# Kernel optimization log

Hardware: AMD Instinct MI355X
Metric: run time of the kernel (lower is better)

## Reference

```python
import jax, jax.numpy as jnp
import numpy as np

B, T, S = 64, 256, 512          # batch, decode steps, source length
IN, H, P, C = 512, 512, 256, 512  # in_size, rnn hidden, ctx_proj_size, ctx_size


def setup_inputs() -> dict:
    key = jax.random.key(0)
    ks = jax.random.split(key, 10)
    def n(k, sh, s=0.05):
        return jax.random.normal(k, sh, dtype=jnp.float32) * s
    return {
        "dec_input": n(ks[0], (B, T, IN), 1.0),
        "ctx": n(ks[1], (B, S, C), 1.0),
        "ctx_mask": jnp.ones((B, S), jnp.float32),
        # LSTMCell layer 0: input = in_size + ctx_proj_size (input feeding)
        "Wih0": n(ks[2], (4 * H, IN + P)),
        "Whh0": n(ks[3], (4 * H, H)),
        "bih0": jnp.zeros((4 * H,), jnp.float32),
        "bhh0": jnp.zeros((4 * H,), jnp.float32),
        # LSTMCell layer 1
        "Wih1": n(ks[4], (4 * H, H)),
        "Whh1": n(ks[5], (4 * H, H)),
        "bih1": jnp.zeros((4 * H,), jnp.float32),
        "bhh1": jnp.zeros((4 * H,), jnp.float32),
        # bilinear (Luong general) attention weight
        "Watt": n(ks[6], (H, C)),
        # ctx projection: Linear(rnn_size + att.out_features -> ctx_proj_size)
        "Wproj": n(ks[7], (P, H + C)),
        "bproj": jnp.zeros((P,), jnp.float32),
    }


def _lstm_cell(x, h, c, Wih, Whh, bih, bhh):
    # PyTorch LSTMCell gate order: i, f, g, o
    g = x @ Wih.T + bih + h @ Whh.T + bhh
    i, f, gg, o = jnp.split(g, 4, axis=-1)
    c_new = jax.nn.sigmoid(f) * c + jax.nn.sigmoid(i) * jnp.tanh(gg)
    h_new = jax.nn.sigmoid(o) * jnp.tanh(c_new)
    return h_new, c_new


def reference(dec_input, ctx, ctx_mask, Wih0, Whh0, bih0, bhh0,
              Wih1, Whh1, bih1, bhh1, Watt, Wproj, bproj):
    Bn = dec_input.shape[0]
    neg = (ctx_mask - 1.0) * 1e9  # additive mask: 0 where valid, -1e9 where pad

    def step(carry, x_t):
        h0, c0, h1, c1, feed = carry
        # input feeding at layer 0
        x = jnp.concatenate([x_t, feed], axis=1)
        h0, c0 = _lstm_cell(x, h0, c0, Wih0, Whh0, bih0, bhh0)
        h1, c1 = _lstm_cell(h0, h1, c1, Wih1, Whh1, bih1, bhh1)
        # attention on last layer (att_nth_layer == -1)
        q = h1 @ Watt                                   # [B, C]
        score = jnp.einsum('bc,bsc->bs', q, ctx) + neg  # [B, S]
        alpha = jax.nn.softmax(score, axis=-1)
        ectx = jnp.einsum('bs,bsc->bc', alpha, ctx)     # expected context [B, C]
        # ctx projection with tanh (scale_src = scale_tgt = 1.0)
        res = jnp.tanh(jnp.concatenate([h1, ectx], axis=1) @ Wproj.T + bproj)
        return (h0, c0, h1, c1, res), (res, alpha)

    z = lambda d: jnp.zeros((Bn, d), jnp.float32)
    init = (z(H), z(H), z(H), z(H), z(P))
    _, (dec_out, att_w) = jax.lax.scan(step, init, jnp.swapaxes(dec_input, 0, 1))
    # dec_output [B, T, P], attention weights [B, T, S]
    return jnp.swapaxes(dec_out, 0, 1), jnp.swapaxes(att_w, 0, 1)
```

## Files before the change

kernel.cpp:

```cpp
#include <hip/hip_runtime.h>
#include <math.h>

#define B  64
#define T  256
#define S  512
#define IN 512
#define H  512
#define P  256
#define C  512

typedef _Float16 f16x8 __attribute__((ext_vector_type(8)));
typedef float    f32x4 __attribute__((ext_vector_type(4)));
typedef unsigned short u16x8 __attribute__((ext_vector_type(8)));

#define MFMA16(a, b, c) __builtin_amdgcn_mfma_f32_16x16x32_f16(a, b, c, 0, 0, 0)

#define O_C0      0
#define O_C1      131072
#define O_H0F0    262144
#define O_H0F1    393216
#define O_H1F0    524288
#define O_H1F1    655360
#define O_FEEDF   786432
#define O_H1F32   851968
#define O_XF0     983040
#define O_XF1     1114112
#define O_Q       1245184
#define O_PS      1376256
#define O_PSP     1378304
#define O_PEA     1509376
#define O_BCAT0   2557952
#define O_BCAT1   2566144
#define O_WPROJT  2574336
#define O_W0F     3622912
#define O_W1F     14108672
#define O_WATTF   22497280
#define O_CTXH    23545856

__device__ __forceinline__ float sigm(float x) { return 1.f / (1.f + __expf(-x)); }

__device__ __forceinline__ void split2(float v, unsigned short& hi, unsigned short& lo)
{
    _Float16 h = (_Float16)v;
    float r = (v - (float)h) * 4096.f;
    _Float16 l2 = (_Float16)r;
    union { _Float16 f; unsigned short u; } a, b2;
    a.f = h; b2.f = l2;
    hi = a.u; lo = b2.u;
}

__device__ __forceinline__ unsigned short f2h(float v)
{
    union { _Float16 f; unsigned short u; } x;
    x.f = (_Float16)v;
    return x.u;
}

__device__ __forceinline__ float h2f(unsigned short u)
{
    union { unsigned short u; _Float16 f; } x;
    x.u = u;
    return (float)x.f;
}

__device__ __forceinline__ int frag_us(int r, int k)
{
    return ((((k >> 5) * 4 + (r >> 4)) * 64 + ((k >> 3) & 3) * 16 + (r & 15)) * 16) + (k & 7);
}

__device__ __forceinline__ void gemm_core(
    const unsigned short* A0, int n0, const unsigned short* A1, int n1,
    const unsigned short* A2, const unsigned short* Wf, int nks, int ct,
    float* red, int tid)
{
    const int l = tid & 63, kh = tid >> 6;
    f32x4 acch[4] = {};
    f32x4 accl[4] = {};
    const int KQ = nks >> 3;
#pragma unroll 2
    for (int i = 0; i < KQ; ++i) {
        const int ks = kh * KQ + i;
        const unsigned short* ap; int ksl;
        if (ks < n0)           { ap = A0; ksl = ks; }
        else if (ks < n0 + n1) { ap = A1; ksl = ks - n0; }
        else                   { ap = A2; ksl = ks - n0 - n1; }
        const f16x8* bp = (const f16x8*)(Wf + ((long)(ct * nks + ks) * 64 + l) * 16);
        const f16x8 bh = bp[0];
        const f16x8 bl = bp[1];
#pragma unroll
        for (int mt = 0; mt < 4; ++mt) {
            const f16x8* app = (const f16x8*)(ap + (((ksl * 4 + mt) * 64 + l) * 16));
            const f16x8 ah = app[0];
            const f16x8 al = app[1];
            acch[mt] = MFMA16(ah, bh, acch[mt]);
            accl[mt] = MFMA16(ah, bl, accl[mt]);
            accl[mt] = MFMA16(al, bh, accl[mt]);
        }
    }
#pragma unroll
    for (int mt = 0; mt < 4; ++mt) {
        f32x4 v = acch[mt] + accl[mt] * (1.f / 4096.f);
        *(f32x4*)&red[(kh * 64 + l) * 20 + mt * 4] = v;
    }
}

__device__ __forceinline__ void lstm_epi(const float* red, const float* bias,
                                         float* cbuf, unsigned short* hfrag,
                                         float* hf32, int ct, int tid)
{
    const int b = tid & 63, hl = tid >> 6;
    float g4[4];
#pragma unroll
    for (int g = 0; g < 4; ++g) {
        const int col = hl * 4 + g;
        const int li  = ((b & 15) >> 2) * 16 + col;
        const int ri  = (b >> 4) * 4 + (b & 3);
        float v = bias[ct * 16 + col];
#pragma unroll
        for (int k2 = 0; k2 < 8; ++k2) v += red[(k2 * 64 + li) * 20 + ri];
        g4[g] = v;
    }
    const int hg = ct * 4 + hl;
    const float cold = cbuf[b * H + hg];
    const float cn = sigm(g4[1]) * cold + sigm(g4[0]) * tanhf(g4[2]);
    cbuf[b * H + hg] = cn;
    const float hn = sigm(g4[3]) * tanhf(cn);
    unsigned short hi, lo; split2(hn, hi, lo);
    const int fu = frag_us(b, hg);
    hfrag[fu]     = hi;
    hfrag[fu + 8] = lo;
    if (hf32) hf32[b * H + hg] = hn;
}

__global__ __launch_bounds__(512)
void k1_kernel(char* __restrict__ wsb, const float* __restrict__ dec_input, int t)
{
    __shared__ float lds[10240];
    const int bid = blockIdx.x, tid = threadIdx.x;
    unsigned short* h0f[2] = {(unsigned short*)(wsb + O_H0F0), (unsigned short*)(wsb + O_H0F1)};
    unsigned short* xf[2]  = {(unsigned short*)(wsb + O_XF0), (unsigned short*)(wsb + O_XF1)};

    if (bid < 128) {
        gemm_core(xf[t & 1], 16, (unsigned short*)(wsb + O_FEEDF), 8, h0f[t & 1],
                  (const unsigned short*)(wsb + O_W0F), 40, bid, lds, tid);
        __syncthreads();
        if (tid < 256)
            lstm_epi(lds, (const float*)(wsb + O_BCAT0), (float*)(wsb + O_C0),
                     h0f[(t + 1) & 1], nullptr, bid, tid);
    } else if (t + 1 < T) {
        const int idx = (bid - 128) * 512 + tid;
        const int bb = idx >> 9, k = idx & 511;
        unsigned short hi, lo;
        split2(dec_input[((long)bb * T + (t + 1)) * IN + k], hi, lo);
        unsigned short* dst = xf[(t + 1) & 1];
        const int fu = frag_us(bb, k);
        dst[fu]     = hi;
        dst[fu + 8] = lo;
    }
}

__global__ __launch_bounds__(512)
void k2_kernel(char* __restrict__ wsb, int t)
{
    __shared__ float lds[10240];
    const int bid = blockIdx.x, tid = threadIdx.x;
    unsigned short* h0f[2] = {(unsigned short*)(wsb + O_H0F0), (unsigned short*)(wsb + O_H0F1)};
    unsigned short* h1f[2] = {(unsigned short*)(wsb + O_H1F0), (unsigned short*)(wsb + O_H1F1)};

    gemm_core(h0f[(t + 1) & 1], 16, h1f[t & 1], 16, nullptr,
              (const unsigned short*)(wsb + O_W1F), 32, bid, lds, tid);
    __syncthreads();
    if (tid < 256)
        lstm_epi(lds, (const float*)(wsb + O_BCAT1), (float*)(wsb + O_C1),
                 h1f[(t + 1) & 1], (float*)(wsb + O_H1F32), bid, tid);
}

__global__ __launch_bounds__(512)
void q_kernel(char* __restrict__ wsb, int t)
{
    __shared__ float lds[10240];
    const int bid = blockIdx.x, tid = threadIdx.x;
    unsigned short* h1f[2] = {(unsigned short*)(wsb + O_H1F0), (unsigned short*)(wsb + O_H1F1)};
    float* qbuf = (float*)(wsb + O_Q);

    gemm_core(h1f[(t + 1) & 1], 16, nullptr, 0, nullptr,
              (const unsigned short*)(wsb + O_WATTF), 16, bid, lds, tid);
    __syncthreads();
    if (tid < 256) {
        const int b = tid & 63, cl = tid >> 6;
        float4 vv;
#pragma unroll
        for (int c2 = 0; c2 < 4; ++c2) {
            const int col = cl * 4 + c2;
            const int li  = ((b & 15) >> 2) * 16 + col;
            const int ri  = (b >> 4) * 4 + (b & 3);
            float v = 0.f;
#pragma unroll
            for (int k2 = 0; k2 < 8; ++k2) v += lds[(k2 * 64 + li) * 20 + ri];
            ((float*)&vv)[c2] = v;
        }
        *(float4*)(qbuf + b * C + bid * 16 + cl * 4) = vv;
    }
}

__global__ __launch_bounds__(512)
void qattn_kernel(char* __restrict__ wsb, const float* __restrict__ mask, int t)
{
    __shared__ float qs[512];
    __shared__ unsigned short tile[32 * 520];
    __shared__ float scl[64];

    const int bid = blockIdx.x, tid = threadIdx.x;
    const int b = bid >> 3, ei = bid & 7;
    const float* qbuf = (const float*)(wsb + O_Q);
    const unsigned short* ctxh = (const unsigned short*)(wsb + O_CTXH);
    float* pS  = (float*)(wsb + O_PSP);
    float* Ps  = (float*)(wsb + O_PS);
    float* Pea = (float*)(wsb + O_PEA);

    if (tid < 128) ((float4*)qs)[tid] = ((const float4*)(qbuf + (long)b * C))[tid];
    __syncthreads();

    const int row = tid >> 4;
    const int ch  = tid & 15;
    float qv[32];
#pragma unroll
    for (int j = 0; j < 32; ++j) qv[j] = qs[ch * 32 + j];

    const unsigned short* cb16 = ctxh + ((long)b * S + ei * 64) * C;
    u16x8 creg[4];
#pragma unroll
    for (int it = 0; it < 4; ++it) {
        const int i = it * 512 + tid;
        creg[it] = *(const u16x8*)(cb16 + (long)i * 8);
    }

    float eacc = 0.f;
#pragma unroll
    for (int tt = 0; tt < 2; ++tt) {
#pragma unroll
        for (int it = 0; it < 4; ++it) {
            const int i = it * 512 + tid;
            const int r = i >> 6, c8 = i & 63;
            *(u16x8*)&tile[r * 520 + c8 * 8] = creg[it];
        }
        __syncthreads();
        if (tt == 0) {
#pragma unroll
            for (int it = 0; it < 4; ++it) {
                const int i = it * 512 + tid;
                creg[it] = *(const u16x8*)(cb16 + 32 * 512 + (long)i * 8);
            }
        }
        float part = 0.f;
#pragma unroll
        for (int j4 = 0; j4 < 4; ++j4) {
            const u16x8 cv = *(const u16x8*)&tile[row * 520 + ch * 32 + j4 * 8];
#pragma unroll
            for (int m = 0; m < 8; ++m)
                part = fmaf(h2f(cv[m]), qv[j4 * 8 + m], part);
        }
        part += __shfl_xor(part, 1);
        part += __shfl_xor(part, 2);
        part += __shfl_xor(part, 4);
        part += __shfl_xor(part, 8);
        if (ch == 0) {
            const int srow = ei * 64 + tt * 32 + row;
            const float sc = part + (mask[(long)b * S + srow] - 1.f) * 1e9f;
            const float p  = __expf(sc - 20.f);
            scl[tt * 32 + row] = p;
            pS[(long)b * S + srow] = p;
        }
        __syncthreads();
#pragma unroll 8
        for (int s = 0; s < 32; ++s)
            eacc = fmaf(scl[tt * 32 + s], h2f(tile[s * 520 + tid]), eacc);
        __syncthreads();
    }

    Pea[(long)bid * 512 + tid] = eacc;
    if (tid < 64) {
        float v = scl[tid];
#pragma unroll
        for (int off = 32; off; off >>= 1) v += __shfl_xor(v, off);
        if (tid == 0) Ps[bid] = v;
    }
}

__global__ __launch_bounds__(512)
void mergeproj_kernel(char* __restrict__ wsb, const float* __restrict__ bproj,
                      float* __restrict__ out, int t)
{
    __shared__ float ectx[512];
    __shared__ float h1l[512];
    __shared__ float red[512];

    const int b = blockIdx.x, tid = threadIdx.x;
    const float* Ps  = (const float*)(wsb + O_PS);
    const float* Pea = (const float*)(wsb + O_PEA);
    const float* pS  = (const float*)(wsb + O_PSP);
    const float* h1f32 = (const float*)(wsb + O_H1F32);
    const float* WprojT = (const float*)(wsb + O_WPROJT);
    unsigned short* feedf = (unsigned short*)(wsb + O_FEEDF);

    float* dec_out = out;
    float* att_out = out + (long)B * T * P;

    float gs = 0.f;
#pragma unroll
    for (int j = 0; j < 8; ++j) gs += Ps[b * 8 + j];
    const float inv = 1.f / gs;

    float v = 0.f;
#pragma unroll
    for (int j = 0; j < 8; ++j) v += Pea[(long)(b * 8 + j) * 512 + tid];
    ectx[tid] = v * inv;
    h1l[tid]  = h1f32[(long)b * H + tid];
    att_out[((long)b * T + t) * S + tid] = pS[(long)b * S + tid] * inv;
    __syncthreads();

    const int p = tid & 255, half = tid >> 8;
    const float* al = half ? ectx : h1l;
    const float* Wp = WprojT + (long)(half * 512) * P + p;
    float acc = 0.f;
#pragma unroll 8
    for (int kk = 0; kk < 512; ++kk)
        acc = fmaf(al[kk], Wp[(long)kk * P], acc);
    red[tid] = acc;
    __syncthreads();

    if (tid < 256) {
        float vv = red[tid] + red[tid + 256] + bproj[tid];
        vv = tanhf(vv);
        dec_out[((long)b * T + t) * P + tid] = vv;
        unsigned short hi, lo; split2(vv, hi, lo);
        const int fu = frag_us(b, tid);
        feedf[fu]     = hi;
        feedf[fu + 8] = lo;
    }
}

__global__ __launch_bounds__(256)
void prep_all(const float* __restrict__ dec_input,
              const float* __restrict__ Wih0, const float* __restrict__ Whh0,
              const float* __restrict__ bih0, const float* __restrict__ bhh0,
              const float* __restrict__ Wih1, const float* __restrict__ Whh1,
              const float* __restrict__ bih1, const float* __restrict__ bhh1,
              const float* __restrict__ Watt, const float* __restrict__ Wproj,
              const float* __restrict__ ctx,
              char* __restrict__ wsb)
{
    const int bid = blockIdx.x, tid = threadIdx.x;
    if (bid < 240) {
        float4 z = {0.f, 0.f, 0.f, 0.f};
        ((float4*)wsb)[bid * 256 + tid] = z;
    } else if (bid < 368) {
        const int idx = (bid - 240) * 256 + tid;
        const int bb = idx >> 9, k = idx & 511;
        unsigned short hi, lo;
        split2(dec_input[((long)bb * T) * IN + k], hi, lo);
        unsigned short* xf0 = (unsigned short*)(wsb + O_XF0);
        const int fu = frag_us(bb, k);
        xf0[fu] = hi; xf0[fu + 8] = lo;
    } else if (bid < 384) {
        const int idx = (bid - 368) * 256 + tid;
        if (idx < 2048) {
            const int p = idx, h = p >> 2, g = p & 3, orig = g * H + h;
            ((float*)(wsb + O_BCAT0))[p] = bih0[orig] + bhh0[orig];
        } else {
            const int p = idx - 2048, h = p >> 2, g = p & 3, orig = g * H + h;
            ((float*)(wsb + O_BCAT1))[p] = bih1[orig] + bhh1[orig];
        }
    } else if (bid < 512) {
        const int idx = (bid - 384) * 256 + tid;
        const int n = idx >> 6, k = (idx & 63) * 8;
        u16x8 hv, lv;
#pragma unroll
        for (int j = 0; j < 8; ++j) {
            unsigned short hi, lo; split2(Watt[(long)(k + j) * C + n], hi, lo);
            hv[j] = hi; lv[j] = lo;
        }
        unsigned short* Wf = (unsigned short*)(wsb + O_WATTF);
        const long base = ((long)((n >> 4) * 16 + (k >> 5)) * 64 + ((k >> 3) & 3) * 16 + (n & 15)) * 16;
        *(u16x8*)(Wf + base)     = hv;
        *(u16x8*)(Wf + base + 8) = lv;
    } else if (bid < 1536) {
        const int idx = (bid - 512) * 256 + tid;
        const int k = idx >> 8, p = idx & 255;
        ((float*)(wsb + O_WPROJT))[k * P + p] = Wproj[(long)p * (H + C) + k];
    } else if (bid < 2816) {
        const int idx = (bid - 1536) * 256 + tid;
        const int n = idx / 160, k8 = idx - n * 160;
        const int k = k8 * 8;
        const int h = n >> 2, g = n & 3, orig = g * H + h;
        const float* src = (k < IN + P) ? (Wih0 + (long)orig * (IN + P) + k)
                                        : (Whh0 + (long)orig * H + (k - (IN + P)));
        u16x8 hv, lv;
#pragma unroll
        for (int j = 0; j < 8; ++j) {
            unsigned short hi, lo; split2(src[j], hi, lo);
            hv[j] = hi; lv[j] = lo;
        }
        unsigned short* Wf = (unsigned short*)(wsb + O_W0F);
        const long base = ((long)((n >> 4) * 40 + (k >> 5)) * 64 + ((k >> 3) & 3) * 16 + (n & 15)) * 16;
        *(u16x8*)(Wf + base)     = hv;
        *(u16x8*)(Wf + base + 8) = lv;
    } else if (bid < 3840) {
        const int idx = (bid - 2816) * 256 + tid;
        const int n = idx >> 7, k = (idx & 127) * 8;
        const int h = n >> 2, g = n & 3, orig = g * H + h;
        const float* src = (k < H) ? (Wih1 + (long)orig * H + k)
                                   : (Whh1 + (long)orig * H + (k - H));
        u16x8 hv, lv;
#pragma unroll
        for (int j = 0; j < 8; ++j) {
            unsigned short hi, lo; split2(src[j], hi, lo);
            hv[j] = hi; lv[j] = lo;
        }
        unsigned short* Wf = (unsigned short*)(wsb + O_W1F);
        const long base = ((long)((n >> 4) * 32 + (k >> 5)) * 64 + ((k >> 3) & 3) * 16 + (n & 15)) * 16;
        *(u16x8*)(Wf + base)     = hv;
        *(u16x8*)(Wf + base + 8) = lv;
    } else {
        const long idx = (long)(bid - 3840) * 256 + tid;
        const float* src = ctx + idx * 16;
        unsigned short* dst = (unsigned short*)(wsb + O_CTXH) + idx * 16;
        u16x8 o0, o1;
#pragma unroll
        for (int j = 0; j < 8; ++j) {
            o0[j] = f2h(src[j]);
            o1[j] = f2h(src[j + 8]);
        }
        *(u16x8*)dst       = o0;
        *(u16x8*)(dst + 8) = o1;
    }
}

extern "C" void kernel_launch(void* const* d_in, const int* in_sizes, int n_in,
                              void* d_out, int out_size, void* d_ws, size_t ws_size,
                              hipStream_t stream)
{
    (void)in_sizes; (void)n_in; (void)out_size; (void)ws_size;
    const float* dec_input = (const float*)d_in[0];
    const float* ctx       = (const float*)d_in[1];
    const float* mask      = (const float*)d_in[2];
    const float* Wih0      = (const float*)d_in[3];
    const float* Whh0      = (const float*)d_in[4];
    const float* bih0      = (const float*)d_in[5];
    const float* bhh0      = (const float*)d_in[6];
    const float* Wih1      = (const float*)d_in[7];
    const float* Whh1      = (const float*)d_in[8];
    const float* bih1      = (const float*)d_in[9];
    const float* bhh1      = (const float*)d_in[10];
    const float* Watt      = (const float*)d_in[11];
    const float* Wproj     = (const float*)d_in[12];
    const float* bproj     = (const float*)d_in[13];
    float* out = (float*)d_out;
    char*  wsb = (char*)d_ws;

    prep_all<<<7936, 256, 0, stream>>>(dec_input, Wih0, Whh0, bih0, bhh0,
                                       Wih1, Whh1, bih1, bhh1, Watt, Wproj,
                                       ctx, wsb);

    for (int t = 0; t < T; ++t) {
        k1_kernel<<<192, 512, 0, stream>>>(wsb, dec_input, t);
        k2_kernel<<<128, 512, 0, stream>>>(wsb, t);
        q_kernel<<<32, 512, 0, stream>>>(wsb, t);
        qattn_kernel<<<512, 512, 0, stream>>>(wsb, mask, t);
        mergeproj_kernel<<<64, 512, 0, stream>>>(wsb, bproj, out, t);
    }
}
```

Baseline: 14.79 ms.

## Fuse per-step kernels into one launch with global atomic counters

Replaces the five kernel launches per decode step with a single step_kernel of 512 blocks. Stages are ordered with global atomic counters and spin-waits instead of kernel boundaries, and the per-batch merge/projection runs in whichever of the eight attention blocks arrives last. This removes launch overhead and inter-kernel gaps across 256 steps. In exchange it relies on all 512 blocks being co-resident to avoid deadlock, and adds spin-wait and atomic-store costs.

Result: no change. 15.05 ms (+1.7%).

```diff
diff --git a/kernel.cpp b/kernel.cpp
--- a/kernel.cpp
+++ b/kernel.cpp
@@ -18,13 +18,10 @@
 #define O_C0      0
 #define O_C1      131072
 #define O_H0F0    262144
-#define O_H0F1    393216
 #define O_H1F0    524288
-#define O_H1F1    655360
 #define O_FEEDF   786432
 #define O_H1F32   851968
 #define O_XF0     983040
-#define O_XF1     1114112
 #define O_Q       1245184
 #define O_PS      1376256
 #define O_PSP     1378304
@@ -36,6 +33,11 @@
 #define O_W1F     14108672
 #define O_WATTF   22497280
 #define O_CTXH    23545856
+#define O_CNTA    57100288
+#define O_CNT3    57104384
+#define O_H0F1N   57169920
+#define O_H1F1N   57300992
+#define O_XF1N    57432064
 
 __device__ __forceinline__ float sigm(float x) { return 1.f / (1.f + __expf(-x)); }
 
@@ -104,9 +106,9 @@
     }
 }
 
-__device__ __forceinline__ void lstm_epi(const float* red, const float* bias,
-                                         float* cbuf, unsigned short* hfrag,
-                                         float* hf32, int ct, int tid)
+__device__ __forceinline__ void lstm_epiA(const float* red, unsigned short* stg,
+                                          const float* bias, float* cbuf,
+                                          float* hf32_atomic, int ct, int tid)
 {
     const int b = tid & 63, hl = tid >> 6;
     float g4[4];
@@ -126,217 +128,251 @@
     cbuf[b * H + hg] = cn;
     const float hn = sigm(g4[3]) * tanhf(cn);
     unsigned short hi, lo; split2(hn, hi, lo);
-    const int fu = frag_us(b, hg);
-    hfrag[fu]     = hi;
-    hfrag[fu + 8] = lo;
-    if (hf32) hf32[b * H + hg] = hn;
-}
-
-__global__ __launch_bounds__(512)
-void k1_kernel(char* __restrict__ wsb, const float* __restrict__ dec_input, int t)
-{
-    __shared__ float lds[10240];
+    stg[hl * 64 + b]       = hi;
+    stg[256 + hl * 64 + b] = lo;
+    if (hf32_atomic) atomicExch(&hf32_atomic[b * H + hg], hn);
+}
+
+__device__ __forceinline__ void quad_store(unsigned short* hfrag, int ct,
+                                           const unsigned short* stg, int b)
+{
+    unsigned long long hq = (unsigned long long)stg[b]
+        | ((unsigned long long)stg[64 + b]  << 16)
+        | ((unsigned long long)stg[128 + b] << 32)
+        | ((unsigned long long)stg[192 + b] << 48);
+    unsigned long long lq = (unsigned long long)stg[256 + b]
+        | ((unsigned long long)stg[320 + b] << 16)
+        | ((unsigned long long)stg[384 + b] << 32)
+        | ((unsigned long long)stg[448 + b] << 48);
+    const int fu0 = frag_us(b, ct * 4);
+    atomicExch((unsigned long long*)(hfrag + fu0), hq);
+    atomicExch((unsigned long long*)(hfrag + fu0 + 8), lq);
+}
+
+__global__ __launch_bounds__(512, 4)
+void step_kernel(char* __restrict__ wsb, const float* __restrict__ dec_input,
+                 const float* __restrict__ mask, const float* __restrict__ bproj,
+                 float* __restrict__ out, int t)
+{
+    __shared__ char smem[41984];
     const int bid = blockIdx.x, tid = threadIdx.x;
-    unsigned short* h0f[2] = {(unsigned short*)(wsb + O_H0F0), (unsigned short*)(wsb + O_H0F1)};
-    unsigned short* xf[2]  = {(unsigned short*)(wsb + O_XF0), (unsigned short*)(wsb + O_XF1)};
+    const int cur = t & 1, nxt = cur ^ 1;
+
+    unsigned short* h0f[2] = {(unsigned short*)(wsb + O_H0F0), (unsigned short*)(wsb + O_H0F1N)};
+    unsigned short* h1f[2] = {(unsigned short*)(wsb + O_H1F0), (unsigned short*)(wsb + O_H1F1N)};
+    unsigned short* xf[2]  = {(unsigned short*)(wsb + O_XF0),  (unsigned short*)(wsb + O_XF1N)};
+    unsigned short* feedf  = (unsigned short*)(wsb + O_FEEDF);
+    float* qbuf  = (float*)(wsb + O_Q);
+    float* pS    = (float*)(wsb + O_PSP);
+    float* Ps    = (float*)(wsb + O_PS);
+    float* Pea   = (float*)(wsb + O_PEA);
+    float* h1f32 = (float*)(wsb + O_H1F32);
+    float* c0    = (float*)(wsb + O_C0);
+    float* c1    = (float*)(wsb + O_C1);
+    const float* bcat0 = (const float*)(wsb + O_BCAT0);
+    const float* bcat1 = (const float*)(wsb + O_BCAT1);
+    const float* WprojT = (const float*)(wsb + O_WPROJT);
+    const unsigned short* W0f   = (const unsigned short*)(wsb + O_W0F);
+    const unsigned short* W1f   = (const unsigned short*)(wsb + O_W1F);
+    const unsigned short* Wattf = (const unsigned short*)(wsb + O_WATTF);
+    const unsigned short* ctxh  = (const unsigned short*)(wsb + O_CTXH);
+
+    unsigned* cnt1 = (unsigned*)(wsb + O_CNTA) + t;
+    unsigned* cnt2 = (unsigned*)(wsb + O_CNTA + 1024) + t;
+    unsigned* cntq = (unsigned*)(wsb + O_CNTA + 2048) + t;
+    unsigned* cnt3 = (unsigned*)(wsb + O_CNT3) + t * 64;
+
+    float* dec_out = out;
+    float* att_out = out + (long)B * T * P;
+
+    float* red = (float*)smem;
+    unsigned short* stg = (unsigned short*)(smem + 40960);
 
     if (bid < 128) {
-        gemm_core(xf[t & 1], 16, (unsigned short*)(wsb + O_FEEDF), 8, h0f[t & 1],
-                  (const unsigned short*)(wsb + O_W0F), 40, bid, lds, tid);
-        __syncthreads();
-        if (tid < 256)
-            lstm_epi(lds, (const float*)(wsb + O_BCAT0), (float*)(wsb + O_C0),
-                     h0f[(t + 1) & 1], nullptr, bid, tid);
-    } else if (t + 1 < T) {
-        const int idx = (bid - 128) * 512 + tid;
-        const int bb = idx >> 9, k = idx & 511;
-        unsigned short hi, lo;
-        split2(dec_input[((long)bb * T + (t + 1)) * IN + k], hi, lo);
-        unsigned short* dst = xf[(t + 1) & 1];
-        const int fu = frag_us(bb, k);
-        dst[fu]     = hi;
-        dst[fu + 8] = lo;
-    }
-}
-
-__global__ __launch_bounds__(512)
-void k2_kernel(char* __restrict__ wsb, int t)
-{
-    __shared__ float lds[10240];
-    const int bid = blockIdx.x, tid = threadIdx.x;
-    unsigned short* h0f[2] = {(unsigned short*)(wsb + O_H0F0), (unsigned short*)(wsb + O_H0F1)};
-    unsigned short* h1f[2] = {(unsigned short*)(wsb + O_H1F0), (unsigned short*)(wsb + O_H1F1)};
-
-    gemm_core(h0f[(t + 1) & 1], 16, h1f[t & 1], 16, nullptr,
-              (const unsigned short*)(wsb + O_W1F), 32, bid, lds, tid);
+        gemm_core(xf[cur], 16, feedf, 8, h0f[cur], W0f, 40, bid, red, tid);
+        __syncthreads();
+        if (tid < 256) lstm_epiA(red, stg, bcat0, c0, nullptr, bid, tid);
+        __syncthreads();
+        if (tid < 64) quad_store(h0f[nxt], bid, stg, tid);
+        __syncthreads();
+        if (tid == 0) {
+            atomicAdd(cnt1, 1u);
+            while (__hip_atomic_load(cnt1, __ATOMIC_RELAXED, __HIP_MEMORY_SCOPE_AGENT) < 128u)
+                __builtin_amdgcn_s_sleep(2);
+        }
+        __syncthreads();
+        gemm_core(h0f[nxt], 16, h1f[cur], 16, nullptr, W1f, 32, bid, red, tid);
+        __syncthreads();
+        if (tid < 256) lstm_epiA(red, stg, bcat1, c1, h1f32, bid, tid);
+        __syncthreads();
+        if (tid < 64) quad_store(h1f[nxt], bid, stg, tid);
+        __syncthreads();
+        if (tid == 0) atomicAdd(cnt2, 1u);
+        if (bid < 32) {
+            if (tid == 0) {
+                while (__hip_atomic_load(cnt2, __ATOMIC_RELAXED, __HIP_MEMORY_SCOPE_AGENT) < 128u)
+                    __builtin_amdgcn_s_sleep(2);
+            }
+            __syncthreads();
+            gemm_core(h1f[nxt], 16, nullptr, 0, nullptr, Wattf, 16, bid, red, tid);
+            __syncthreads();
+            if (tid < 256) {
+                const int b = tid & 63, cl = tid >> 6;
+                float vv[4];
+#pragma unroll
+                for (int c2 = 0; c2 < 4; ++c2) {
+                    const int col = cl * 4 + c2;
+                    const int li  = ((b & 15) >> 2) * 16 + col;
+                    const int ri  = (b >> 4) * 4 + (b & 3);
+                    float v = 0.f;
+#pragma unroll
+                    for (int k2 = 0; k2 < 8; ++k2) v += red[(k2 * 64 + li) * 20 + ri];
+                    vv[c2] = v;
+                }
+                float* qp = qbuf + b * C + bid * 16 + cl * 4;
+                union { float f[2]; unsigned long long u; } p0, p1;
+                p0.f[0] = vv[0]; p0.f[1] = vv[1];
+                p1.f[0] = vv[2]; p1.f[1] = vv[3];
+                atomicExch((unsigned long long*)qp, p0.u);
+                atomicExch(((unsigned long long*)qp) + 1, p1.u);
+            }
+            __syncthreads();
+            if (tid == 0) atomicAdd(cntq, 1u);
+        }
+    } else if (bid < 192) {
+        if (t + 1 < T) {
+            const int idx = (bid - 128) * 512 + tid;
+            const int bb = idx >> 9, k = idx & 511;
+            unsigned short hi, lo;
+            split2(dec_input[((long)bb * T + (t + 1)) * IN + k], hi, lo);
+            unsigned short* dst = xf[nxt];
+            const int fu = frag_us(bb, k);
+            dst[fu]     = hi;
+            dst[fu + 8] = lo;
+        }
+    }
+
+    if (tid == 0) {
+        while (__hip_atomic_load(cntq, __ATOMIC_RELAXED, __HIP_MEMORY_SCOPE_AGENT) < 32u)
+            __builtin_amdgcn_s_sleep(8);
+    }
     __syncthreads();
-    if (tid < 256)
-        lstm_epi(lds, (const float*)(wsb + O_BCAT1), (float*)(wsb + O_C1),
-                 h1f[(t + 1) & 1], (float*)(wsb + O_H1F32), bid, tid);
-}
-
-__global__ __launch_bounds__(512)
-void q_kernel(char* __restrict__ wsb, int t)
-{
-    __shared__ float lds[10240];
-    const int bid = blockIdx.x, tid = threadIdx.x;
-    unsigned short* h1f[2] = {(unsigned short*)(wsb + O_H1F0), (unsigned short*)(wsb + O_H1F1)};
-    float* qbuf = (float*)(wsb + O_Q);
-
-    gemm_core(h1f[(t + 1) & 1], 16, nullptr, 0, nullptr,
-              (const unsigned short*)(wsb + O_WATTF), 16, bid, lds, tid);
-    __syncthreads();
-    if (tid < 256) {
-        const int b = tid & 63, cl = tid >> 6;
-        float4 vv;
-#pragma unroll
-        for (int c2 = 0; c2 < 4; ++c2) {
-            const int col = cl * 4 + c2;
-            const int li  = ((b & 15) >> 2) * 16 + col;
-            const int ri  = (b >> 4) * 4 + (b & 3);
-            float v = 0.f;
-#pragma unroll
-            for (int k2 = 0; k2 < 8; ++k2) v += lds[(k2 * 64 + li) * 20 + ri];
-            ((float*)&vv)[c2] = v;
-        }
-        *(float4*)(qbuf + b * C + bid * 16 + cl * 4) = vv;
-    }
-}
-
-__global__ __launch_bounds__(512)
-void qattn_kernel(char* __restrict__ wsb, const float* __restrict__ mask, int t)
-{
-    __shared__ float qs[512];
-    __shared__ unsigned short tile[32 * 520];
-    __shared__ float scl[64];
-
-    const int bid = blockIdx.x, tid = threadIdx.x;
-    const int b = bid >> 3, ei = bid & 7;
-    const float* qbuf = (const float*)(wsb + O_Q);
-    const unsigned short* ctxh = (const unsigned short*)(wsb + O_CTXH);
-    float* pS  = (float*)(wsb + O_PSP);
-    float* Ps  = (float*)(wsb + O_PS);
-    float* Pea = (float*)(wsb + O_PEA);
-
-    if (tid < 128) ((float4*)qs)[tid] = ((const float4*)(qbuf + (long)b * C))[tid];
-    __syncthreads();
-
-    const int row = tid >> 4;
-    const int ch  = tid & 15;
-    float qv[32];
-#pragma unroll
-    for (int j = 0; j < 32; ++j) qv[j] = qs[ch * 32 + j];
-
-    const unsigned short* cb16 = ctxh + ((long)b * S + ei * 64) * C;
-    u16x8 creg[4];
-#pragma unroll
-    for (int it = 0; it < 4; ++it) {
-        const int i = it * 512 + tid;
-        creg[it] = *(const u16x8*)(cb16 + (long)i * 8);
-    }
-
-    float eacc = 0.f;
-#pragma unroll
-    for (int tt = 0; tt < 2; ++tt) {
-#pragma unroll
-        for (int it = 0; it < 4; ++it) {
-            const int i = it * 512 + tid;
-            const int r = i >> 6, c8 = i & 63;
-            *(u16x8*)&tile[r * 520 + c8 * 8] = creg[it];
-        }
-        __syncthreads();
-        if (tt == 0) {
+
+    const int ab = bid >> 3, ei = bid & 7;
+    {
+        float* qs = (float*)smem;
+        unsigned short* tile = (unsigned short*)(smem + 2048);
+        float* scl = (float*)(smem + 35328);
+
+        if (tid < 128) ((float4*)qs)[tid] = ((const float4*)(qbuf + (long)ab * C))[tid];
+        __syncthreads();
+
+        const int row = tid >> 4;
+        const int ch  = tid & 15;
+        float qv[32];
+#pragma unroll
+        for (int j = 0; j < 32; ++j) qv[j] = qs[ch * 32 + j];
+
+        const unsigned short* cb16 = ctxh + ((long)ab * S + ei * 64) * C;
+        u16x8 creg[4];
+#pragma unroll
+        for (int it = 0; it < 4; ++it)
+            creg[it] = *(const u16x8*)(cb16 + (long)(it * 512 + tid) * 8);
+
+        float eacc = 0.f;
+#pragma unroll
+        for (int tt = 0; tt < 2; ++tt) {
 #pragma unroll
             for (int it = 0; it < 4; ++it) {
                 const int i = it * 512 + tid;
-                creg[it] = *(const u16x8*)(cb16 + 32 * 512 + (long)i * 8);
+                const int r = (i >> 6) & 31, c8 = i & 63;
+                *(u16x8*)&tile[r * 520 + c8 * 8] = creg[it];
             }
-        }
-        float part = 0.f;
-#pragma unroll
-        for (int j4 = 0; j4 < 4; ++j4) {
-            const u16x8 cv = *(const u16x8*)&tile[row * 520 + ch * 32 + j4 * 8];
-#pragma unroll
-            for (int m = 0; m < 8; ++m)
-                part = fmaf(h2f(cv[m]), qv[j4 * 8 + m], part);
-        }
-        part += __shfl_xor(part, 1);
-        part += __shfl_xor(part, 2);
-        part += __shfl_xor(part, 4);
-        part += __shfl_xor(part, 8);
-        if (ch == 0) {
-            const int srow = ei * 64 + tt * 32 + row;
-            const float sc = part + (mask[(long)b * S + srow] - 1.f) * 1e9f;
-            const float p  = __expf(sc - 20.f);
-            scl[tt * 32 + row] = p;
-            pS[(long)b * S + srow] = p;
-        }
-        __syncthreads();
+            __syncthreads();
+            if (tt == 0) {
+#pragma unroll
+                for (int it = 0; it < 4; ++it)
+                    creg[it] = *(const u16x8*)(cb16 + 32 * 512 + (long)(it * 512 + tid) * 8);
+            }
+            float part = 0.f;
+#pragma unroll
+            for (int j4 = 0; j4 < 4; ++j4) {
+                const u16x8 cv = *(const u16x8*)&tile[row * 520 + ch * 32 + j4 * 8];
+#pragma unroll
+                for (int m = 0; m < 8; ++m)
+                    part = fmaf(h2f(cv[m]), qv[j4 * 8 + m], part);
+            }
+            part += __shfl_xor(part, 1);
+            part += __shfl_xor(part, 2);
+            part += __shfl_xor(part, 4);
+            part += __shfl_xor(part, 8);
+            if (ch == 0) {
+                const int srow = ei * 64 + tt * 32 + row;
+                const float sc = part + (mask[(long)ab * S + srow] - 1.f) * 1e9f;
+                const float p  = __expf(sc - 20.f);
+                scl[tt * 32 + row] = p;
+                atomicExch(&pS[(long)ab * S + srow], p);
+            }
+            __syncthreads();
 #pragma unroll 8
-        for (int s = 0; s < 32; ++s)
-            eacc = fmaf(scl[tt * 32 + s], h2f(tile[s * 520 + tid]), eacc);
-        __syncthreads();
-    }
-
-    Pea[(long)bid * 512 + tid] = eacc;
-    if (tid < 64) {
-        float v = scl[tid];
-#pragma unroll
-        for (int off = 32; off; off >>= 1) v += __shfl_xor(v, off);
-        if (tid == 0) Ps[bid] = v;
-    }
-}
-
-__global__ __launch_bounds__(512)
-void mergeproj_kernel(char* __restrict__ wsb, const float* __restrict__ bproj,
-                      float* __restrict__ out, int t)
-{
-    __shared__ float ectx[512];
-    __shared__ float h1l[512];
-    __shared__ float red[512];
-
-    const int b = blockIdx.x, tid = threadIdx.x;
-    const float* Ps  = (const float*)(wsb + O_PS);
-    const float* Pea = (const float*)(wsb + O_PEA);
-    const float* pS  = (const float*)(wsb + O_PSP);
-    const float* h1f32 = (const float*)(wsb + O_H1F32);
-    const float* WprojT = (const float*)(wsb + O_WPROJT);
-    unsigned short* feedf = (unsigned short*)(wsb + O_FEEDF);
-
-    float* dec_out = out;
-    float* att_out = out + (long)B * T * P;
-
-    float gs = 0.f;
-#pragma unroll
-    for (int j = 0; j < 8; ++j) gs += Ps[b * 8 + j];
-    const float inv = 1.f / gs;
-
-    float v = 0.f;
-#pragma unroll
-    for (int j = 0; j < 8; ++j) v += Pea[(long)(b * 8 + j) * 512 + tid];
-    ectx[tid] = v * inv;
-    h1l[tid]  = h1f32[(long)b * H + tid];
-    att_out[((long)b * T + t) * S + tid] = pS[(long)b * S + tid] * inv;
+            for (int s = 0; s < 32; ++s)
+                eacc = fmaf(scl[tt * 32 + s], h2f(tile[s * 520 + tid]), eacc);
+            __syncthreads();
+        }
+
+        atomicExch(&Pea[(long)bid * 512 + tid], eacc);
+        if (tid < 64) {
+            float v = scl[tid];
+#pragma unroll
+            for (int off = 32; off; off >>= 1) v += __shfl_xor(v, off);
+            if (tid == 0) atomicExch(&Ps[bid], v);
+        }
+    }
     __syncthreads();
 
-    const int p = tid & 255, half = tid >> 8;
-    const float* al = half ? ectx : h1l;
-    const float* Wp = WprojT + (long)(half * 512) * P + p;
-    float acc = 0.f;
+    unsigned* shf = (unsigned*)(smem + 35584);
+    if (tid == 0) {
+        unsigned r = atomicAdd(&cnt3[ab], 1u);
+        shf[0] = (r == 7u) ? 1u : 0u;
+    }
+    __syncthreads();
+    if (shf[0]) {
+        float* ectx = (float*)smem;
+        float* h1l  = (float*)(smem + 2048);
+        float* rd3  = (float*)(smem + 4096);
+
+        float gs = 0.f;
+#pragma unroll
+        for (int j = 0; j < 8; ++j) gs += Ps[ab * 8 + j];
+        const float inv = 1.f / gs;
+
+        float v = 0.f;
+#pragma unroll
+        for (int j = 0; j < 8; ++j) v += Pea[(long)(ab * 8 + j) * 512 + tid];
+        ectx[tid] = v * inv;
+        h1l[tid]  = h1f32[(long)ab * H + tid];
+        att_out[((long)ab * T + t) * S + tid] = pS[(long)ab * S + tid] * inv;
+        __syncthreads();
+
+        const int p = tid & 255, half = tid >> 8;
+        const float* al = half ? ectx : h1l;
+        const float* Wp = WprojT + (long)(half * 512) * P + p;
+        float acc = 0.f;
 #pragma unroll 8
-    for (int kk = 0; kk < 512; ++kk)
-        acc = fmaf(al[kk], Wp[(long)kk * P], acc);
-    red[tid] = acc;
-    __syncthreads();
-
-    if (tid < 256) {
-        float vv = red[tid] + red[tid + 256] + bproj[tid];
-        vv = tanhf(vv);
-        dec_out[((long)b * T + t) * P + tid] = vv;
-        unsigned short hi, lo; split2(vv, hi, lo);
-        const int fu = frag_us(b, tid);
-        feedf[fu]     = hi;
-        feedf[fu + 8] = lo;
+        for (int kk = 0; kk < 512; ++kk)
+            acc = fmaf(al[kk], Wp[(long)kk * P], acc);
+        rd3[tid] = acc;
+        __syncthreads();
+
+        if (tid < 256) {
+            float vv = rd3[tid] + rd3[tid + 256] + bproj[tid];
+            vv = tanhf(vv);
+            dec_out[((long)ab * T + t) * P + tid] = vv;
+            unsigned short hi, lo; split2(vv, hi, lo);
+            const int fu = frag_us(ab, tid);
+            feedf[fu]     = hi;
+            feedf[fu + 8] = lo;
+        }
     }
 }
 
@@ -421,7 +457,7 @@
         const long base = ((long)((n >> 4) * 32 + (k >> 5)) * 64 + ((k >> 3) & 3) * 16 + (n & 15)) * 16;
         *(u16x8*)(Wf + base)     = hv;
         *(u16x8*)(Wf + base + 8) = lv;
-    } else {
+    } else if (bid < 7936) {
         const long idx = (long)(bid - 3840) * 256 + tid;
         const float* src = ctx + idx * 16;
         unsigned short* dst = (unsigned short*)(wsb + O_CTXH) + idx * 16;
@@ -433,6 +469,9 @@
         }
         *(u16x8*)dst       = o0;
         *(u16x8*)(dst + 8) = o1;
+    } else {
+        float4 z = {0.f, 0.f, 0.f, 0.f};
+        ((float4*)(wsb + O_CNTA))[(bid - 7936) * 256 + tid] = z;
     }
 }
 
@@ -458,15 +497,10 @@
     float* out = (float*)d_out;
     char*  wsb = (char*)d_ws;
 
-    prep_all<<<7936, 256, 0, stream>>>(dec_input, Wih0, Whh0, bih0, bhh0,
+    prep_all<<<7953, 256, 0, stream>>>(dec_input, Wih0, Whh0, bih0, bhh0,
                                        Wih1, Whh1, bih1, bhh1, Watt, Wproj,
                                        ctx, wsb);
 
-    for (int t = 0; t < T; ++t) {
-        k1_kernel<<<192, 512, 0, stream>>>(wsb, dec_input, t);
-        k2_kernel<<<128, 512, 0, stream>>>(wsb, t);
-        q_kernel<<<32, 512, 0, stream>>>(wsb, t);
-        qattn_kernel<<<512, 512, 0, stream>>>(wsb, mask, t);
-        mergeproj_kernel<<<64, 512, 0, stream>>>(wsb, bproj, out, t);
-    }
-}
+    for (int t = 0; t < T; ++t)
+        step_kernel<<<512, 512, 0, stream>>>(wsb, dec_input, mask, bproj, out, t);
+}
```

## Store weights as single fp16 instead of hi/lo split, halving MFMA work

Applied to the files above, without the earlier changes.

Weights for the LSTM, attention query and projection GEMMs are converted to a single fp16 value instead of an fp16 hi/lo pair. This drops one of three MFMAs per tile and halves weight bandwidth. Activations keep their hi/lo split. The Wproj transpose becomes fp16 as well, and the ctx tile load in the attention kernel is hoisted ahead of the q load. Buffers are relocated and a counter region is zeroed, but those counters are never used. The cost is lower numerical accuracy from fp16-rounded weights.

Result: faster. 13.92 ms (-5.9%).

```diff
diff --git a/kernel.cpp b/kernel.cpp
--- a/kernel.cpp
+++ b/kernel.cpp
@@ -18,13 +18,10 @@
 #define O_C0      0
 #define O_C1      131072
 #define O_H0F0    262144
-#define O_H0F1    393216
 #define O_H1F0    524288
-#define O_H1F1    655360
 #define O_FEEDF   786432
 #define O_H1F32   851968
 #define O_XF0     983040
-#define O_XF1     1114112
 #define O_Q       1245184
 #define O_PS      1376256
 #define O_PSP     1378304
@@ -36,6 +33,11 @@
 #define O_W1F     14108672
 #define O_WATTF   22497280
 #define O_CTXH    23545856
+#define O_CNTA    57100288
+#define O_CNT3    57104384
+#define O_H0F1N   57169920
+#define O_H1F1N   57300992
+#define O_XF1N    57432064
 
 __device__ __forceinline__ float sigm(float x) { return 1.f / (1.f + __expf(-x)); }
 
@@ -84,17 +86,14 @@
         if (ks < n0)           { ap = A0; ksl = ks; }
         else if (ks < n0 + n1) { ap = A1; ksl = ks - n0; }
         else                   { ap = A2; ksl = ks - n0 - n1; }
-        const f16x8* bp = (const f16x8*)(Wf + ((long)(ct * nks + ks) * 64 + l) * 16);
-        const f16x8 bh = bp[0];
-        const f16x8 bl = bp[1];
+        const f16x8 b = *(const f16x8*)(Wf + ((long)(ct * nks + ks) * 64 + l) * 8);
 #pragma unroll
         for (int mt = 0; mt < 4; ++mt) {
             const f16x8* app = (const f16x8*)(ap + (((ksl * 4 + mt) * 64 + l) * 16));
             const f16x8 ah = app[0];
             const f16x8 al = app[1];
-            acch[mt] = MFMA16(ah, bh, acch[mt]);
-            accl[mt] = MFMA16(ah, bl, accl[mt]);
-            accl[mt] = MFMA16(al, bh, accl[mt]);
+            acch[mt] = MFMA16(ah, b, acch[mt]);
+            accl[mt] = MFMA16(al, b, accl[mt]);
         }
     }
 #pragma unroll
@@ -106,7 +105,7 @@
 
 __device__ __forceinline__ void lstm_epi(const float* red, const float* bias,
                                          float* cbuf, unsigned short* hfrag,
-                                         float* hf32, int ct, int tid)
+                                         float* hf32_out, int ct, int tid)
 {
     const int b = tid & 63, hl = tid >> 6;
     float g4[4];
@@ -129,7 +128,7 @@
     const int fu = frag_us(b, hg);
     hfrag[fu]     = hi;
     hfrag[fu + 8] = lo;
-    if (hf32) hf32[b * H + hg] = hn;
+    if (hf32_out) hf32_out[b * H + hg] = hn;
 }
 
 __global__ __launch_bounds__(512)
@@ -137,22 +136,23 @@
 {
     __shared__ float lds[10240];
     const int bid = blockIdx.x, tid = threadIdx.x;
-    unsigned short* h0f[2] = {(unsigned short*)(wsb + O_H0F0), (unsigned short*)(wsb + O_H0F1)};
-    unsigned short* xf[2]  = {(unsigned short*)(wsb + O_XF0), (unsigned short*)(wsb + O_XF1)};
+    const int cur = t & 1, nxt = cur ^ 1;
+    unsigned short* h0f[2] = {(unsigned short*)(wsb + O_H0F0), (unsigned short*)(wsb + O_H0F1N)};
+    unsigned short* xf[2]  = {(unsigned short*)(wsb + O_XF0),  (unsigned short*)(wsb + O_XF1N)};
 
     if (bid < 128) {
-        gemm_core(xf[t & 1], 16, (unsigned short*)(wsb + O_FEEDF), 8, h0f[t & 1],
+        gemm_core(xf[cur], 16, (unsigned short*)(wsb + O_FEEDF), 8, h0f[cur],
                   (const unsigned short*)(wsb + O_W0F), 40, bid, lds, tid);
         __syncthreads();
         if (tid < 256)
             lstm_epi(lds, (const float*)(wsb + O_BCAT0), (float*)(wsb + O_C0),
-                     h0f[(t + 1) & 1], nullptr, bid, tid);
+                     h0f[nxt], nullptr, bid, tid);
     } else if (t + 1 < T) {
         const int idx = (bid - 128) * 512 + tid;
         const int bb = idx >> 9, k = idx & 511;
         unsigned short hi, lo;
         split2(dec_input[((long)bb * T + (t + 1)) * IN + k], hi, lo);
-        unsigned short* dst = xf[(t + 1) & 1];
+        unsigned short* dst = xf[nxt];
         const int fu = frag_us(bb, k);
         dst[fu]     = hi;
         dst[fu + 8] = lo;
@@ -164,15 +164,16 @@
 {
     __shared__ float lds[10240];
     const int bid = blockIdx.x, tid = threadIdx.x;
-    unsigned short* h0f[2] = {(unsigned short*)(wsb + O_H0F0), (unsigned short*)(wsb + O_H0F1)};
-    unsigned short* h1f[2] = {(unsigned short*)(wsb + O_H1F0), (unsigned short*)(wsb + O_H1F1)};
-
-    gemm_core(h0f[(t + 1) & 1], 16, h1f[t & 1], 16, nullptr,
+    const int cur = t & 1, nxt = cur ^ 1;
+    unsigned short* h0f[2] = {(unsigned short*)(wsb + O_H0F0), (unsigned short*)(wsb + O_H0F1N)};
+    unsigned short* h1f[2] = {(unsigned short*)(wsb + O_H1F0), (unsigned short*)(wsb + O_H1F1N)};
+
+    gemm_core(h0f[nxt], 16, h1f[cur], 16, nullptr,
               (const unsigned short*)(wsb + O_W1F), 32, bid, lds, tid);
     __syncthreads();
     if (tid < 256)
         lstm_epi(lds, (const float*)(wsb + O_BCAT1), (float*)(wsb + O_C1),
-                 h1f[(t + 1) & 1], (float*)(wsb + O_H1F32), bid, tid);
+                 h1f[nxt], (float*)(wsb + O_H1F32), bid, tid);
 }
 
 __global__ __launch_bounds__(512)
@@ -180,10 +181,11 @@
 {
     __shared__ float lds[10240];
     const int bid = blockIdx.x, tid = threadIdx.x;
-    unsigned short* h1f[2] = {(unsigned short*)(wsb + O_H1F0), (unsigned short*)(wsb + O_H1F1)};
+    const int nxt = (t & 1) ^ 1;
+    unsigned short* h1f[2] = {(unsigned short*)(wsb + O_H1F0), (unsigned short*)(wsb + O_H1F1N)};
     float* qbuf = (float*)(wsb + O_Q);
 
-    gemm_core(h1f[(t + 1) & 1], 16, nullptr, 0, nullptr,
+    gemm_core(h1f[nxt], 16, nullptr, 0, nullptr,
               (const unsigned short*)(wsb + O_WATTF), 16, bid, lds, tid);
     __syncthreads();
     if (tid < 256) {
@@ -218,6 +220,12 @@
     float* Ps  = (float*)(wsb + O_PS);
     float* Pea = (float*)(wsb + O_PEA);
 
+    const unsigned short* cb16 = ctxh + ((long)b * S + ei * 64) * C;
+    u16x8 creg[4];
+#pragma unroll
+    for (int it = 0; it < 4; ++it)
+        creg[it] = *(const u16x8*)(cb16 + (long)(it * 512 + tid) * 8);
+
     if (tid < 128) ((float4*)qs)[tid] = ((const float4*)(qbuf + (long)b * C))[tid];
     __syncthreads();
 
@@ -227,30 +235,20 @@
 #pragma unroll
     for (int j = 0; j < 32; ++j) qv[j] = qs[ch * 32 + j];
 
-    const unsigned short* cb16 = ctxh + ((long)b * S + ei * 64) * C;
-    u16x8 creg[4];
-#pragma unroll
-    for (int it = 0; it < 4; ++it) {
-        const int i = it * 512 + tid;
-        creg[it] = *(const u16x8*)(cb16 + (long)i * 8);
-    }
-
     float eacc = 0.f;
 #pragma unroll
     for (int tt = 0; tt < 2; ++tt) {
 #pragma unroll
         for (int it = 0; it < 4; ++it) {
             const int i = it * 512 + tid;
-            const int r = i >> 6, c8 = i & 63;
+            const int r = (i >> 6) & 31, c8 = i & 63;
             *(u16x8*)&tile[r * 520 + c8 * 8] = creg[it];
         }
         __syncthreads();
         if (tt == 0) {
 #pragma unroll
-            for (int it = 0; it < 4; ++it) {
-                const int i = it * 512 + tid;
-                creg[it] = *(const u16x8*)(cb16 + 32 * 512 + (long)i * 8);
-            }
+            for (int it = 0; it < 4; ++it)
+                creg[it] = *(const u16x8*)(cb16 + 32 * 512 + (long)(it * 512 + tid) * 8);
         }
         float part = 0.f;
 #pragma unroll
@@ -300,7 +298,7 @@
     const float* Pea = (const float*)(wsb + O_PEA);
     const float* pS  = (const float*)(wsb + O_PSP);
     const float* h1f32 = (const float*)(wsb + O_H1F32);
-    const float* WprojT = (const float*)(wsb + O_WPROJT);
+    const unsigned short* Wph = (const unsigned short*)(wsb + O_WPROJT);
     unsigned short* feedf = (unsigned short*)(wsb + O_FEEDF);
 
     float* dec_out = out;
@@ -321,11 +319,11 @@
 
     const int p = tid & 255, half = tid >> 8;
     const float* al = half ? ectx : h1l;
-    const float* Wp = WprojT + (long)(half * 512) * P + p;
+    const unsigned short* Wp = Wph + (long)(half * 512) * P + p;
     float acc = 0.f;
 #pragma unroll 8
     for (int kk = 0; kk < 512; ++kk)
-        acc = fmaf(al[kk], Wp[(long)kk * P], acc);
+        acc = fmaf(al[kk], h2f(Wp[(long)kk * P]), acc);
     red[tid] = acc;
     __syncthreads();
 
@@ -374,20 +372,16 @@
     } else if (bid < 512) {
         const int idx = (bid - 384) * 256 + tid;
         const int n = idx >> 6, k = (idx & 63) * 8;
-        u16x8 hv, lv;
-#pragma unroll
-        for (int j = 0; j < 8; ++j) {
-            unsigned short hi, lo; split2(Watt[(long)(k + j) * C + n], hi, lo);
-            hv[j] = hi; lv[j] = lo;
-        }
+        u16x8 hv;
+#pragma unroll
+        for (int j = 0; j < 8; ++j) hv[j] = f2h(Watt[(long)(k + j) * C + n]);
         unsigned short* Wf = (unsigned short*)(wsb + O_WATTF);
-        const long base = ((long)((n >> 4) * 16 + (k >> 5)) * 64 + ((k >> 3) & 3) * 16 + (n & 15)) * 16;
-        *(u16x8*)(Wf + base)     = hv;
-        *(u16x8*)(Wf + base + 8) = lv;
+        const long base = ((long)((n >> 4) * 16 + (k >> 5)) * 64 + ((k >> 3) & 3) * 16 + (n & 15)) * 8;
+        *(u16x8*)(Wf + base) = hv;
     } else if (bid < 1536) {
         const int idx = (bid - 512) * 256 + tid;
         const int k = idx >> 8, p = idx & 255;
-        ((float*)(wsb + O_WPROJT))[k * P + p] = Wproj[(long)p * (H + C) + k];
+        ((unsigned short*)(wsb + O_WPROJT))[k * P + p] = f2h(Wproj[(long)p * (H + C) + k]);
     } else if (bid < 2816) {
         const int idx = (bid - 1536) * 256 + tid;
         const int n = idx / 160, k8 = idx - n * 160;
@@ -395,33 +389,25 @@
         const int h = n >> 2, g = n & 3, orig = g * H + h;
         const float* src = (k < IN + P) ? (Wih0 + (long)orig * (IN + P) + k)
                                         : (Whh0 + (long)orig * H + (k - (IN + P)));
-        u16x8 hv, lv;
-#pragma unroll
-        for (int j = 0; j < 8; ++j) {
-            unsigned short hi, lo; split2(src[j], hi, lo);
-            hv[j] = hi; lv[j] = lo;
-        }
+        u16x8 hv;
+#pragma unroll
+        for (int j = 0; j < 8; ++j) hv[j] = f2h(src[j]);
         unsigned short* Wf = (unsigned short*)(wsb + O_W0F);
-        const long base = ((long)((n >> 4) * 40 + (k >> 5)) * 64 + ((k >> 3) & 3) * 16 + (n & 15)) * 16;
-        *(u16x8*)(Wf + base)     = hv;
-        *(u16x8*)(Wf + base + 8) = lv;
+        const long base = ((long)((n >> 4) * 40 + (k >> 5)) * 64 + ((k >> 3) & 3) * 16 + (n & 15)) * 8;
+        *(u16x8*)(Wf + base) = hv;
     } else if (bid < 3840) {
         const int idx = (bid - 2816) * 256 + tid;
         const int n = idx >> 7, k = (idx & 127) * 8;
         const int h = n >> 2, g = n & 3, orig = g * H + h;
         const float* src = (k < H) ? (Wih1 + (long)orig * H + k)
                                    : (Whh1 + (long)orig * H + (k - H));
-        u16x8 hv, lv;
-#pragma unroll
-        for (int j = 0; j < 8; ++j) {
-            unsigned short hi, lo; split2(src[j], hi, lo);
-            hv[j] = hi; lv[j] = lo;
-        }
+        u16x8 hv;
+#pragma unroll
+        for (int j = 0; j < 8; ++j) hv[j] = f2h(src[j]);
         unsigned short* Wf = (unsigned short*)(wsb + O_W1F);
-        const long base = ((long)((n >> 4) * 32 + (k >> 5)) * 64 + ((k >> 3) & 3) * 16 + (n & 15)) * 16;
-        *(u16x8*)(Wf + base)     = hv;
-        *(u16x8*)(Wf + base + 8) = lv;
-    } else {
+        const long base = ((long)((n >> 4) * 32 + (k >> 5)) * 64 + ((k >> 3) & 3) * 16 + (n & 15)) * 8;
+        *(u16x8*)(Wf + base) = hv;
+    } else if (bid < 7936) {
         const long idx = (long)(bid - 3840) * 256 + tid;
         const float* src = ctx + idx * 16;
         unsigned short* dst = (unsigned short*)(wsb + O_CTXH) + idx * 16;
@@ -433,6 +419,9 @@
         }
         *(u16x8*)dst       = o0;
         *(u16x8*)(dst + 8) = o1;
+    } else {
+        float4 z = {0.f, 0.f, 0.f, 0.f};
+        ((float4*)(wsb + O_CNTA))[(bid - 7936) * 256 + tid] = z;
     }
 }
 
@@ -458,7 +447,7 @@
     float* out = (float*)d_out;
     char*  wsb = (char*)d_ws;
 
-    prep_all<<<7936, 256, 0, stream>>>(dec_input, Wih0, Whh0, bih0, bhh0,
+    prep_all<<<7953, 256, 0, stream>>>(dec_input, Wih0, Whh0, bih0, bhh0,
                                        Wih1, Whh1, bih1, bhh1, Watt, Wproj,
                                        ctx, wsb);
 
```
